# Optimization experiments

Measured on AMD Instinct MI355X. Metric: run time of the kernel, lower is better.

The kernel has to match this reference:

```python
import jax, jax.numpy as jnp
import numpy as np

B, N, HD, U = 2, 512, 64, 128  # batch, nodes, h_dim, mlp width


def _init(key, shape):
    return jax.random.normal(key, shape, dtype=jnp.float32) / np.sqrt(shape[0]).astype(np.float32)


def setup_inputs() -> dict:
    key = jax.random.key(0)
    ks = jax.random.split(key, 12)
    x = jax.random.normal(ks[0], (B, N, 3), dtype=jnp.float32)
    h = jax.random.normal(ks[1], (B, N, HD), dtype=jnp.float32)
    p = {}
    p['We1'] = _init(ks[2], (1 + 2 * HD, U)); p['be1'] = jnp.zeros((U,), jnp.float32)
    p['We2'] = _init(ks[3], (U, U));          p['be2'] = jnp.zeros((U,), jnp.float32)
    p['Winf'] = _init(ks[4], (U, 1));         p['binf'] = jnp.zeros((1,), jnp.float32)
    p['Wx1'] = _init(ks[5], (U, U));          p['bx1'] = jnp.zeros((U,), jnp.float32)
    p['Wx2'] = _init(ks[6], (U, U));          p['bx2'] = jnp.zeros((U,), jnp.float32)
    p['Wx3'] = _init(ks[7], (U, 1));          p['bx3'] = jnp.zeros((1,), jnp.float32)
    p['Wh1'] = _init(ks[8], (U + HD, U));     p['bh1'] = jnp.zeros((U,), jnp.float32)
    p['Wh2'] = _init(ks[9], (U, U));          p['bh2'] = jnp.zeros((U,), jnp.float32)
    p['Wout'] = _init(ks[10], (U, HD));       p['bout'] = jnp.zeros((HD,), jnp.float32)
    return {'x': x, 'h': h, **p}


def _mlp2(t, W1, b1, W2, b2):
    # hk.nets.MLP([U, U], activation=elu), activate_final=False
    return jax.nn.elu(t @ W1 + b1) @ W2 + b2


def reference(x, h, We1, be1, We2, be2, Winf, binf, Wx1, bx1, Wx2, bx2, Wx3, bx3, Wh1, bh1, Wh2, bh2, Wout, bout):
    Bn, Nn, _ = x.shape
    hd = h.shape[-1]
    mask = 1.0 - jnp.eye(Nn, dtype=x.dtype)  # zero the i==j diagonal
    # diff[b,i,j] = x[b,j] - x[b,i]  (matches x - x[:, None] in the original)
    diff = (x[:, None, :, :] - x[:, :, None, :]) * mask[None, :, :, None]  # [B,N,N,3]
    sq = jnp.sum(diff * diff, axis=-1)
    norms = jnp.sqrt(jnp.where(mask > 0, sq, 1.0)) * mask  # safe sqrt; diag exactly 0
    # h_combos[b,i,j] = concat(h[b,j], h[b,i])
    h_j = jnp.broadcast_to(h[:, None, :, :], (Bn, Nn, Nn, hd))
    h_i = jnp.broadcast_to(h[:, :, None, :], (Bn, Nn, Nn, hd))
    feat = jnp.concatenate([norms[..., None], h_j, h_i], axis=-1)  # [B,N,N,1+2*hd]
    m_ij = _mlp2(feat, We1, be1, We2, be2) * mask[None, :, :, None]  # [B,N,N,U]
    e = jax.nn.sigmoid(m_ij @ Winf + binf)[..., 0] * mask            # [B,N,N]
    m_i = jnp.einsum('bijd,bij->bid', m_ij, e)                       # [B,N,U]
    # phi_x: MLP(activate_final=True) then Linear(1)
    hid = jax.nn.elu(jax.nn.elu(m_ij @ Wx1 + bx1) @ Wx2 + bx2)
    phi_x_out = (hid @ Wx3 + bx3)[..., 0] * mask                     # [B,N,N]
    shift = jnp.einsum('bijd,bij->bid', diff, phi_x_out) / (Nn - 1)  # [B,N,3]
    h_new = _mlp2(jnp.concatenate([m_i, h], axis=-1), Wh1, bh1, Wh2, bh2) @ Wout + bout
    return (x + shift, h_new)
```

## Files before the change

kernel.cpp:

```cpp
#include <hip/hip_runtime.h>
#include <math.h>


#define BB    2
#define NN    512
#define HDIM  64
#define UDIM  128
#define JT    64
#define NTILE (NN / JT)
#define FP    72
#define PP    136

typedef float f32x4 __attribute__((ext_vector_type(4)));
typedef short s16x8 __attribute__((ext_vector_type(8)));

__device__ __forceinline__ ushort f2bf(float f) {
    union { float f; unsigned u; } v; v.f = f;
    return (ushort)((v.u + 0x7FFFu + ((v.u >> 16) & 1u)) >> 16);
}
__device__ __forceinline__ float bf2f(ushort s) {
    union { unsigned u; float f; } v; v.u = ((unsigned)s) << 16; return v.f;
}
__device__ __forceinline__ unsigned pk2(float lo, float hi) {
    unsigned r;
    asm("v_cvt_pk_bf16_f32 %0, %1, %2" : "=v"(r) : "v"(lo), "v"(hi));
    return r;
}
__device__ __forceinline__ f32x4 MFMA(s16x8 a, s16x8 b, f32x4 c) {
    return __builtin_amdgcn_mfma_f32_16x16x32_bf16(a, b, c, 0, 0, 0);
}
__device__ __forceinline__ float eluf(float v) { return v > 0.f ? v : __expf(v) - 1.f; }

__device__ __forceinline__ void load_wfrags(const float* __restrict__ W, int q, int uc0,
                                            s16x8 (&dst)[4][2]) {
#pragma unroll
    for (int s = 0; s < 4; ++s)
#pragma unroll
        for (int n = 0; n < 2; ++n) {
            s16x8 r;
#pragma unroll
            for (int ii = 0; ii < 8; ++ii)
                r[ii] = (short)f2bf(W[(32 * s + 8 * q + ii) * UDIM + uc0 + n]);
            dst[s][n] = r;
        }
}

template <int KSTEPS, int PITCH>
__device__ __forceinline__ void gemm_P(const ushort* __restrict__ P, const s16x8 (&wB)[KSTEPS][2],
                                       int l15, int q, f32x4 (&acc)[4][2]) {
#pragma unroll
    for (int s = 0; s < KSTEPS; ++s) {
        s16x8 a[4];
#pragma unroll
        for (int m = 0; m < 4; ++m)
            a[m] = *(const s16x8*)(P + (16 * m + l15) * PITCH + 32 * s + 8 * q);
#pragma unroll
        for (int m = 0; m < 4; ++m) {
            acc[m][0] = MFMA(a[m], wB[s][0], acc[m][0]);
            acc[m][1] = MFMA(a[m], wB[s][1], acc[m][1]);
        }
    }
}

template <bool ELU>
__device__ __forceinline__ void store_P(ushort* __restrict__ P, const f32x4 (&v)[4][2],
                                        int q, int uc0) {
#pragma unroll
    for (int m = 0; m < 4; ++m)
#pragma unroll
        for (int r = 0; r < 4; ++r) {
            const int row = 16 * m + 4 * q + r;
            float a = v[m][0][r], c = v[m][1][r];
            if (ELU) { a = eluf(a); c = eluf(c); }
            *(unsigned*)(P + row * PP + uc0) = pk2(a, c);
        }
}

__global__ __launch_bounds__(256, 2) void egnn_mfma(
    const float* __restrict__ x, const float* __restrict__ h,
    const float* __restrict__ We1, const float* __restrict__ be1,
    const float* __restrict__ We2, const float* __restrict__ be2,
    const float* __restrict__ Winf, const float* __restrict__ binf,
    const float* __restrict__ Wx1, const float* __restrict__ bx1,
    const float* __restrict__ Wx2, const float* __restrict__ bx2,
    const float* __restrict__ Wx3, const float* __restrict__ bx3,
    const float* __restrict__ Wh1, const float* __restrict__ bh1,
    const float* __restrict__ Wh2, const float* __restrict__ bh2,
    const float* __restrict__ Wout, const float* __restrict__ bout,
    float* __restrict__ out) {
    __shared__ ushort F[JT][FP];
    __shared__ ushort P1[JT][PP];
    __shared__ ushort P2[JT][PP];
    __shared__ float normL[JT];
    __shared__ float diffL[JT][3];
    __shared__ float rpartE[4][JT];
    __shared__ float rpartP[4][JT];
    __shared__ float eL[JT];
    __shared__ float bias1L[UDIM];
    __shared__ float WinfL[UDIM], Wx3L[UDIM];
    __shared__ float catL[UDIM + HDIM];
    __shared__ float th1[UDIM], th2[UDIM];

    const int bi = blockIdx.x;
    const int b  = bi >> 9;
    const int i  = bi & (NN - 1);
    const int tid  = threadIdx.x;
    const int lane = tid & 63;
    const int w    = tid >> 6;
    const int l15  = lane & 15;
    const int q    = lane >> 4;
    const int uc0  = 32 * w + 2 * l15;

    s16x8 wB1[2][2];
#pragma unroll
    for (int s = 0; s < 2; ++s)
#pragma unroll
        for (int n = 0; n < 2; ++n) {
            s16x8 r;
#pragma unroll
            for (int ii = 0; ii < 8; ++ii)
                r[ii] = (short)f2bf(We1[(1 + 32 * s + 8 * q + ii) * UDIM + uc0 + n]);
            wB1[s][n] = r;
        }
    s16x8 wB2[4][2], wB3[4][2], wB4[4][2];
    load_wfrags(We2, q, uc0, wB2);
    load_wfrags(Wx1, q, uc0, wB3);
    load_wfrags(Wx2, q, uc0, wB4);

    if (tid < UDIM) {
        WinfL[tid] = Winf[tid];
        Wx3L[tid]  = Wx3[tid];
        float s = be1[tid];
        const float* hi = &h[(b * NN + i) * HDIM];
#pragma unroll 8
        for (int k = 0; k < HDIM; ++k)
            s = fmaf(hi[k], We1[(1 + HDIM + k) * UDIM + tid], s);
        bias1L[tid] = s;
    }
    const float w0n0 = We1[uc0], w0n1 = We1[uc0 + 1];
    const float b2n0 = be2[uc0], b2n1 = be2[uc0 + 1];
    const float bqn0 = bx1[uc0], bqn1 = bx1[uc0 + 1];
    const float brn0 = bx2[uc0], brn1 = bx2[uc0 + 1];
    const float binf0 = binf[0], bx30 = bx3[0];
    const float xi0 = x[(b * NN + i) * 3 + 0];
    const float xi1 = x[(b * NN + i) * 3 + 1];
    const float xi2 = x[(b * NN + i) * 3 + 2];
    __syncthreads();
    const float b1n0 = bias1L[uc0], b1n1 = bias1L[uc0 + 1];

    float mi0 = 0.f, mi1 = 0.f;
    float sh0 = 0.f, sh1 = 0.f, sh2 = 0.f;

    for (int t = 0; t < NTILE; ++t) {
        const int j0 = t * JT;
        __syncthreads();

        {
            const int jr = tid >> 2, k0 = (tid & 3) * 16;
            const float* hp = &h[(b * NN + j0 + jr) * HDIM + k0];
            const float4 f0 = *(const float4*)hp;
            const float4 f1 = *(const float4*)(hp + 4);
            const float4 f2 = *(const float4*)(hp + 8);
            const float4 f3 = *(const float4*)(hp + 12);
            uint4 pv0, pv1;
            pv0.x = pk2(f0.x, f0.y); pv0.y = pk2(f0.z, f0.w);
            pv0.z = pk2(f1.x, f1.y); pv0.w = pk2(f1.z, f1.w);
            pv1.x = pk2(f2.x, f2.y); pv1.y = pk2(f2.z, f2.w);
            pv1.z = pk2(f3.x, f3.y); pv1.w = pk2(f3.z, f3.w);
            *(uint4*)&F[jr][k0]     = pv0;
            *(uint4*)&F[jr][k0 + 8] = pv1;
        }
        if (tid < JT) {
            const int j = j0 + tid;
            float d0 = x[(b * NN + j) * 3 + 0] - xi0;
            float d1 = x[(b * NN + j) * 3 + 1] - xi1;
            float d2 = x[(b * NN + j) * 3 + 2] - xi2;
            if (j == i) { d0 = 0.f; d1 = 0.f; d2 = 0.f; }
            diffL[tid][0] = d0; diffL[tid][1] = d1; diffL[tid][2] = d2;
            normL[tid] = (j == i) ? 0.f : sqrtf(d0 * d0 + d1 * d1 + d2 * d2);
        }
        __syncthreads();

        f32x4 acc[4][2];
#pragma unroll
        for (int m = 0; m < 4; ++m)
#pragma unroll
            for (int r = 0; r < 4; ++r) {
                const float nrm = normL[16 * m + 4 * q + r];
                acc[m][0][r] = fmaf(nrm, w0n0, b1n0);
                acc[m][1][r] = fmaf(nrm, w0n1, b1n1);
            }
        gemm_P<2, FP>(&F[0][0], wB1, l15, q, acc);
        store_P<true>(&P1[0][0], acc, q, uc0);
        __syncthreads();

        f32x4 macc[4][2];
#pragma unroll
        for (int m = 0; m < 4; ++m)
#pragma unroll
            for (int r = 0; r < 4; ++r) { macc[m][0][r] = b2n0; macc[m][1][r] = b2n1; }
        gemm_P<4, PP>(&P1[0][0], wB2, l15, q, macc);
#pragma unroll
        for (int m = 0; m < 4; ++m)
#pragma unroll
            for (int r = 0; r < 4; ++r)
                if (j0 + 16 * m + 4 * q + r == i) { macc[m][0][r] = 0.f; macc[m][1][r] = 0.f; }
        store_P<false>(&P2[0][0], macc, q, uc0);
        __syncthreads();

        {
            const int jj = tid & 63, sl = tid >> 6;
            const ushort* pr = &P2[jj][32 * sl];
            float p = 0.f;
#pragma unroll
            for (int cc = 0; cc < 4; ++cc) {
                const s16x8 mv = *(const s16x8*)(pr + 8 * cc);
#pragma unroll
                for (int c = 0; c < 8; ++c)
                    p = fmaf(bf2f((ushort)mv[c]), WinfL[32 * sl + 8 * cc + c], p);
            }
            rpartE[sl][jj] = p;
        }
        f32x4 qacc[4][2];
#pragma unroll
        for (int m = 0; m < 4; ++m)
#pragma unroll
            for (int r = 0; r < 4; ++r) { qacc[m][0][r] = bqn0; qacc[m][1][r] = bqn1; }
        gemm_P<4, PP>(&P2[0][0], wB3, l15, q, qacc);
        store_P<true>(&P1[0][0], qacc, q, uc0);
        __syncthreads();

        if (tid < JT) {
            float s = rpartE[0][tid] + rpartE[1][tid] + rpartE[2][tid] + rpartE[3][tid];
            float e = 1.f / (1.f + __expf(-(s + binf0)));
            if (j0 + tid == i) e = 0.f;
            eL[tid] = e;
        }
        f32x4 racc[4][2];
#pragma unroll
        for (int m = 0; m < 4; ++m)
#pragma unroll
            for (int r = 0; r < 4; ++r) { racc[m][0][r] = brn0; racc[m][1][r] = brn1; }
        gemm_P<4, PP>(&P1[0][0], wB4, l15, q, racc);
        store_P<true>(&P2[0][0], racc, q, uc0);
        __syncthreads();

        {
            const int jj = tid & 63, sl = tid >> 6;
            const ushort* pr = &P2[jj][32 * sl];
            float p = 0.f;
#pragma unroll
            for (int cc = 0; cc < 4; ++cc) {
                const s16x8 mv = *(const s16x8*)(pr + 8 * cc);
#pragma unroll
                for (int c = 0; c < 8; ++c)
                    p = fmaf(bf2f((ushort)mv[c]), Wx3L[32 * sl + 8 * cc + c], p);
            }
            rpartP[sl][jj] = p;
        }
#pragma unroll
        for (int m = 0; m < 4; ++m)
#pragma unroll
            for (int r = 0; r < 4; ++r) {
                const float e = eL[16 * m + 4 * q + r];
                mi0 = fmaf(macc[m][0][r], e, mi0);
                mi1 = fmaf(macc[m][1][r], e, mi1);
            }
        __syncthreads();

        if (tid < JT) {
            float s = rpartP[0][tid] + rpartP[1][tid] + rpartP[2][tid] + rpartP[3][tid];
            s += bx30;
            if (j0 + tid == i) s = 0.f;
            float v0 = diffL[tid][0] * s;
            float v1 = diffL[tid][1] * s;
            float v2 = diffL[tid][2] * s;
#pragma unroll
            for (int d = 1; d < 64; d <<= 1) {
                v0 += __shfl_xor(v0, d);
                v1 += __shfl_xor(v1, d);
                v2 += __shfl_xor(v2, d);
            }
            sh0 += v0; sh1 += v1; sh2 += v2;
        }
    }

    __syncthreads();
    {
        float v0 = mi0, v1 = mi1;
        v0 += __shfl_xor(v0, 16); v0 += __shfl_xor(v0, 32);
        v1 += __shfl_xor(v1, 16); v1 += __shfl_xor(v1, 32);
        if (lane < 16) {
            catL[uc0]     = v0;
            catL[uc0 + 1] = v1;
        }
    }
    if (tid >= 128 && tid < 128 + HDIM)
        catL[UDIM + tid - 128] = h[(b * NN + i) * HDIM + (tid - 128)];
    if (tid == 0) {
        const float inv = 1.f / (float)(NN - 1);
        out[(b * NN + i) * 3 + 0] = x[(b * NN + i) * 3 + 0] + sh0 * inv;
        out[(b * NN + i) * 3 + 1] = x[(b * NN + i) * 3 + 1] + sh1 * inv;
        out[(b * NN + i) * 3 + 2] = x[(b * NN + i) * 3 + 2] + sh2 * inv;
    }
    __syncthreads();

    if (tid < UDIM) {
        float s = bh1[tid];
        for (int k = 0; k < UDIM + HDIM; ++k) s = fmaf(catL[k], Wh1[k * UDIM + tid], s);
        th1[tid] = eluf(s);
    }
    __syncthreads();
    if (tid < UDIM) {
        float s = bh2[tid];
        for (int k = 0; k < UDIM; ++k) s = fmaf(th1[k], Wh2[k * UDIM + tid], s);
        th2[tid] = s;
    }
    __syncthreads();
    if (tid < HDIM) {
        float s = bout[tid];
        for (int k = 0; k < UDIM; ++k) s = fmaf(th2[k], Wout[k * HDIM + tid], s);
        out[BB * NN * 3 + (b * NN + i) * HDIM + tid] = s;
    }
}

extern "C" void kernel_launch(void* const* d_in, const int* in_sizes, int n_in,
                              void* d_out, int out_size, void* d_ws, size_t ws_size,
                              hipStream_t stream) {
    const float* x    = (const float*)d_in[0];
    const float* h    = (const float*)d_in[1];
    const float* We1  = (const float*)d_in[2];
    const float* be1  = (const float*)d_in[3];
    const float* We2  = (const float*)d_in[4];
    const float* be2  = (const float*)d_in[5];
    const float* Winf = (const float*)d_in[6];
    const float* binf = (const float*)d_in[7];
    const float* Wx1  = (const float*)d_in[8];
    const float* bx1  = (const float*)d_in[9];
    const float* Wx2  = (const float*)d_in[10];
    const float* bx2  = (const float*)d_in[11];
    const float* Wx3  = (const float*)d_in[12];
    const float* bx3  = (const float*)d_in[13];
    const float* Wh1  = (const float*)d_in[14];
    const float* bh1  = (const float*)d_in[15];
    const float* Wh2  = (const float*)d_in[16];
    const float* bh2  = (const float*)d_in[17];
    const float* Wout = (const float*)d_in[18];
    const float* bout = (const float*)d_in[19];
    float* out = (float*)d_out;

    hipLaunchKernelGGL(egnn_mfma, dim3(BB * NN), dim3(256), 0, stream,
                       x, h, We1, be1, We2, be2, Winf, binf, Wx1, bx1, Wx2, bx2,
                       Wx3, bx3, Wh1, bh1, Wh2, bh2, Wout, bout, out);
}
```

Before: 141.2 us.

## Double-buffer j-tiles, fold norm and Winf projection into MFMA, cut barriers

Prefetches the next tile's h rows and coordinate differences into registers during the current tile's GEMMs, then writes them into a double-buffered LDS tile. The norm term moves into an extra K-step of the first MFMA GEMM, and the Winf edge projection rides on wave 0's Wx1 GEMM as an extra MFMA column. The Wx3 projection is reduced in registers with shuffles instead of a separate LDS pass. This removes two barriers per tile and the scalar bf16 dot-product loops. In exchange it adds register pressure, makes wave 0 do more work than the others, and rounds the norm to bf16.

After: 418.4 us. 196% more time.

```diff
diff --git a/kernel.cpp b/kernel.cpp
--- a/kernel.cpp
+++ b/kernel.cpp
@@ -18,9 +18,6 @@
     union { float f; unsigned u; } v; v.f = f;
     return (ushort)((v.u + 0x7FFFu + ((v.u >> 16) & 1u)) >> 16);
 }
-__device__ __forceinline__ float bf2f(ushort s) {
-    union { unsigned u; float f; } v; v.u = ((unsigned)s) << 16; return v.f;
-}
 __device__ __forceinline__ unsigned pk2(float lo, float hi) {
     unsigned r;
     asm("v_cvt_pk_bf16_f32 %0, %1, %2" : "=v"(r) : "v"(lo), "v"(hi));
@@ -45,9 +42,11 @@
         }
 }
 
-template <int KSTEPS, int PITCH>
-__device__ __forceinline__ void gemm_P(const ushort* __restrict__ P, const s16x8 (&wB)[KSTEPS][2],
-                                       int l15, int q, f32x4 (&acc)[4][2]) {
+template <int KSTEPS, int PITCH, bool EXTRA>
+__device__ __forceinline__ void gemm_P(const ushort* __restrict__ P,
+                                       const s16x8 (&wB)[KSTEPS][2], const s16x8* wE,
+                                       int l15, int q, f32x4 (&acc)[4][2], f32x4* eacc) {
+    __builtin_amdgcn_s_setprio(1);
 #pragma unroll
     for (int s = 0; s < KSTEPS; ++s) {
         s16x8 a[4];
@@ -58,8 +57,10 @@
         for (int m = 0; m < 4; ++m) {
             acc[m][0] = MFMA(a[m], wB[s][0], acc[m][0]);
             acc[m][1] = MFMA(a[m], wB[s][1], acc[m][1]);
-        }
-    }
+            if (EXTRA) eacc[m] = MFMA(a[m], wE[s], eacc[m]);
+        }
+    }
+    __builtin_amdgcn_s_setprio(0);
 }
 
 template <bool ELU>
@@ -88,16 +89,14 @@
     const float* __restrict__ Wh2, const float* __restrict__ bh2,
     const float* __restrict__ Wout, const float* __restrict__ bout,
     float* __restrict__ out) {
-    __shared__ ushort F[JT][FP];
+    __shared__ ushort F[2][JT + 1][FP];
     __shared__ ushort P1[JT][PP];
     __shared__ ushort P2[JT][PP];
-    __shared__ float normL[JT];
-    __shared__ float diffL[JT][3];
-    __shared__ float rpartE[4][JT];
-    __shared__ float rpartP[4][JT];
+    __shared__ float diffL[2][JT][3];
+    __shared__ float rp3[4][JT];
     __shared__ float eL[JT];
     __shared__ float bias1L[UDIM];
-    __shared__ float WinfL[UDIM], Wx3L[UDIM];
+    __shared__ float shiftL[3];
     __shared__ float catL[UDIM + HDIM];
     __shared__ float th1[UDIM], th2[UDIM];
 
@@ -110,8 +109,9 @@
     const int l15  = lane & 15;
     const int q    = lane >> 4;
     const int uc0  = 32 * w + 2 * l15;
-
-    s16x8 wB1[2][2];
+    const int jr   = tid >> 2, k0 = (tid & 3) * 16;
+
+    s16x8 wB1[3][2];
 #pragma unroll
     for (int s = 0; s < 2; ++s)
 #pragma unroll
@@ -122,14 +122,29 @@
                 r[ii] = (short)f2bf(We1[(1 + 32 * s + 8 * q + ii) * UDIM + uc0 + n]);
             wB1[s][n] = r;
         }
+#pragma unroll
+    for (int n = 0; n < 2; ++n) {
+        s16x8 r;
+#pragma unroll
+        for (int ii = 0; ii < 8; ++ii)
+            r[ii] = (q == 0 && ii == 0) ? (short)f2bf(We1[uc0 + n]) : (short)0;
+        wB1[2][n] = r;
+    }
     s16x8 wB2[4][2], wB3[4][2], wB4[4][2];
     load_wfrags(We2, q, uc0, wB2);
     load_wfrags(Wx1, q, uc0, wB3);
     load_wfrags(Wx2, q, uc0, wB4);
+    s16x8 wE[4];
+#pragma unroll
+    for (int s = 0; s < 4; ++s) {
+        s16x8 r;
+#pragma unroll
+        for (int ii = 0; ii < 8; ++ii)
+            r[ii] = (l15 == 0) ? (short)f2bf(Winf[32 * s + 8 * q + ii]) : (short)0;
+        wE[s] = r;
+    }
 
     if (tid < UDIM) {
-        WinfL[tid] = Winf[tid];
-        Wx3L[tid]  = Wx3[tid];
         float s = be1[tid];
         const float* hi = &h[(b * NN + i) * HDIM];
 #pragma unroll 8
@@ -137,60 +152,77 @@
             s = fmaf(hi[k], We1[(1 + HDIM + k) * UDIM + tid], s);
         bias1L[tid] = s;
     }
-    const float w0n0 = We1[uc0], w0n1 = We1[uc0 + 1];
     const float b2n0 = be2[uc0], b2n1 = be2[uc0 + 1];
     const float bqn0 = bx1[uc0], bqn1 = bx1[uc0 + 1];
     const float brn0 = bx2[uc0], brn1 = bx2[uc0 + 1];
+    const float wx30 = Wx3[uc0], wx31 = Wx3[uc0 + 1];
     const float binf0 = binf[0], bx30 = bx3[0];
     const float xi0 = x[(b * NN + i) * 3 + 0];
     const float xi1 = x[(b * NN + i) * 3 + 1];
     const float xi2 = x[(b * NN + i) * 3 + 2];
-    __syncthreads();
-    const float b1n0 = bias1L[uc0], b1n1 = bias1L[uc0 + 1];
-
-    float mi0 = 0.f, mi1 = 0.f;
-    float sh0 = 0.f, sh1 = 0.f, sh2 = 0.f;
-
-    for (int t = 0; t < NTILE; ++t) {
-        const int j0 = t * JT;
-        __syncthreads();
-
-        {
-            const int jr = tid >> 2, k0 = (tid & 3) * 16;
-            const float* hp = &h[(b * NN + j0 + jr) * HDIM + k0];
-            const float4 f0 = *(const float4*)hp;
-            const float4 f1 = *(const float4*)(hp + 4);
-            const float4 f2 = *(const float4*)(hp + 8);
-            const float4 f3 = *(const float4*)(hp + 12);
-            uint4 pv0, pv1;
-            pv0.x = pk2(f0.x, f0.y); pv0.y = pk2(f0.z, f0.w);
-            pv0.z = pk2(f1.x, f1.y); pv0.w = pk2(f1.z, f1.w);
-            pv1.x = pk2(f2.x, f2.y); pv1.y = pk2(f2.z, f2.w);
-            pv1.z = pk2(f3.x, f3.y); pv1.w = pk2(f3.z, f3.w);
-            *(uint4*)&F[jr][k0]     = pv0;
-            *(uint4*)&F[jr][k0 + 8] = pv1;
-        }
+
+    if (tid < 2 * FP) {
+        const int f = tid / FP, c = tid % FP;
+        F[f][JT][c] = 0;
+    }
+    {
+        const float* hp = &h[(b * NN + jr) * HDIM + k0];
+        const float4 f0 = *(const float4*)hp;
+        const float4 f1 = *(const float4*)(hp + 4);
+        const float4 f2 = *(const float4*)(hp + 8);
+        const float4 f3 = *(const float4*)(hp + 12);
+        uint4 pv0, pv1;
+        pv0.x = pk2(f0.x, f0.y); pv0.y = pk2(f0.z, f0.w);
+        pv0.z = pk2(f1.x, f1.y); pv0.w = pk2(f1.z, f1.w);
+        pv1.x = pk2(f2.x, f2.y); pv1.y = pk2(f2.z, f2.w);
+        pv1.z = pk2(f3.x, f3.y); pv1.w = pk2(f3.z, f3.w);
+        *(uint4*)&F[0][jr][k0]     = pv0;
+        *(uint4*)&F[0][jr][k0 + 8] = pv1;
         if (tid < JT) {
-            const int j = j0 + tid;
+            const int j = tid;
             float d0 = x[(b * NN + j) * 3 + 0] - xi0;
             float d1 = x[(b * NN + j) * 3 + 1] - xi1;
             float d2 = x[(b * NN + j) * 3 + 2] - xi2;
             if (j == i) { d0 = 0.f; d1 = 0.f; d2 = 0.f; }
-            diffL[tid][0] = d0; diffL[tid][1] = d1; diffL[tid][2] = d2;
-            normL[tid] = (j == i) ? 0.f : sqrtf(d0 * d0 + d1 * d1 + d2 * d2);
-        }
-        __syncthreads();
-
+            diffL[0][tid][0] = d0; diffL[0][tid][1] = d1; diffL[0][tid][2] = d2;
+            const float nrm = sqrtf(d0 * d0 + d1 * d1 + d2 * d2);
+            s16x8 nr = {(short)f2bf(nrm), 0, 0, 0, 0, 0, 0, 0};
+            *(s16x8*)&F[0][tid][64] = nr;
+        }
+    }
+    __syncthreads();
+    const float b1n0 = bias1L[uc0], b1n1 = bias1L[uc0 + 1];
+
+    float mi0 = 0.f, mi1 = 0.f;
+    float shc = 0.f;
+
+    for (int t = 0; t < NTILE; ++t) {
+        const int cur = t & 1, nxt = cur ^ 1;
+        const int j0 = t * JT;
+        const bool more = (t + 1 < NTILE);
+
+        float4 hv0, hv1, hv2, hv3;
+        float sxd0 = 0.f, sxd1 = 0.f, sxd2 = 0.f;
+        if (more) {
+            const float* hp = &h[(b * NN + j0 + JT + jr) * HDIM + k0];
+            hv0 = *(const float4*)hp;
+            hv1 = *(const float4*)(hp + 4);
+            hv2 = *(const float4*)(hp + 8);
+            hv3 = *(const float4*)(hp + 12);
+            if (tid < JT) {
+                const int j = j0 + JT + tid;
+                sxd0 = x[(b * NN + j) * 3 + 0] - xi0;
+                sxd1 = x[(b * NN + j) * 3 + 1] - xi1;
+                sxd2 = x[(b * NN + j) * 3 + 2] - xi2;
+                if (j == i) { sxd0 = 0.f; sxd1 = 0.f; sxd2 = 0.f; }
+            }
+        }
         f32x4 acc[4][2];
 #pragma unroll
         for (int m = 0; m < 4; ++m)
 #pragma unroll
-            for (int r = 0; r < 4; ++r) {
-                const float nrm = normL[16 * m + 4 * q + r];
-                acc[m][0][r] = fmaf(nrm, w0n0, b1n0);
-                acc[m][1][r] = fmaf(nrm, w0n1, b1n1);
-            }
-        gemm_P<2, FP>(&F[0][0], wB1, l15, q, acc);
+            for (int r = 0; r < 4; ++r) { acc[m][0][r] = b1n0; acc[m][1][r] = b1n1; }
+        gemm_P<3, FP, false>(&F[cur][0][0], wB1, nullptr, l15, q, acc, nullptr);
         store_P<true>(&P1[0][0], acc, q, uc0);
         __syncthreads();
 
@@ -199,7 +231,7 @@
         for (int m = 0; m < 4; ++m)
 #pragma unroll
             for (int r = 0; r < 4; ++r) { macc[m][0][r] = b2n0; macc[m][1][r] = b2n1; }
-        gemm_P<4, PP>(&P1[0][0], wB2, l15, q, macc);
+        gemm_P<4, PP, false>(&P1[0][0], wB2, nullptr, l15, q, macc, nullptr);
 #pragma unroll
         for (int m = 0; m < 4; ++m)
 #pragma unroll
@@ -208,56 +240,50 @@
         store_P<false>(&P2[0][0], macc, q, uc0);
         __syncthreads();
 
-        {
-            const int jj = tid & 63, sl = tid >> 6;
-            const ushort* pr = &P2[jj][32 * sl];
-            float p = 0.f;
-#pragma unroll
-            for (int cc = 0; cc < 4; ++cc) {
-                const s16x8 mv = *(const s16x8*)(pr + 8 * cc);
-#pragma unroll
-                for (int c = 0; c < 8; ++c)
-                    p = fmaf(bf2f((ushort)mv[c]), WinfL[32 * sl + 8 * cc + c], p);
-            }
-            rpartE[sl][jj] = p;
-        }
         f32x4 qacc[4][2];
 #pragma unroll
         for (int m = 0; m < 4; ++m)
 #pragma unroll
             for (int r = 0; r < 4; ++r) { qacc[m][0][r] = bqn0; qacc[m][1][r] = bqn1; }
-        gemm_P<4, PP>(&P2[0][0], wB3, l15, q, qacc);
+        if (w == 0) {
+            f32x4 eacc[4];
+#pragma unroll
+            for (int m = 0; m < 4; ++m)
+#pragma unroll
+                for (int r = 0; r < 4; ++r) eacc[m][r] = 0.f;
+            gemm_P<4, PP, true>(&P2[0][0], wB3, wE, l15, q, qacc, eacc);
+            if (l15 == 0) {
+#pragma unroll
+                for (int m = 0; m < 4; ++m)
+#pragma unroll
+                    for (int r = 0; r < 4; ++r) {
+                        const int row = 16 * m + 4 * q + r;
+                        float e = 1.f / (1.f + __expf(-(eacc[m][r] + binf0)));
+                        if (j0 + row == i) e = 0.f;
+                        eL[row] = e;
+                    }
+            }
+        } else {
+            gemm_P<4, PP, false>(&P2[0][0], wB3, nullptr, l15, q, qacc, nullptr);
+        }
         store_P<true>(&P1[0][0], qacc, q, uc0);
+        if (more) {
+            uint4 pv0, pv1;
+            pv0.x = pk2(hv0.x, hv0.y); pv0.y = pk2(hv0.z, hv0.w);
+            pv0.z = pk2(hv1.x, hv1.y); pv0.w = pk2(hv1.z, hv1.w);
+            pv1.x = pk2(hv2.x, hv2.y); pv1.y = pk2(hv2.z, hv2.w);
+            pv1.z = pk2(hv3.x, hv3.y); pv1.w = pk2(hv3.z, hv3.w);
+            *(uint4*)&F[nxt][jr][k0]     = pv0;
+            *(uint4*)&F[nxt][jr][k0 + 8] = pv1;
+            if (tid < JT) {
+                diffL[nxt][tid][0] = sxd0; diffL[nxt][tid][1] = sxd1; diffL[nxt][tid][2] = sxd2;
+                const float nrm = sqrtf(sxd0 * sxd0 + sxd1 * sxd1 + sxd2 * sxd2);
+                s16x8 nr = {(short)f2bf(nrm), 0, 0, 0, 0, 0, 0, 0};
+                *(s16x8*)&F[nxt][tid][64] = nr;
+            }
+        }
         __syncthreads();
 
-        if (tid < JT) {
-            float s = rpartE[0][tid] + rpartE[1][tid] + rpartE[2][tid] + rpartE[3][tid];
-            float e = 1.f / (1.f + __expf(-(s + binf0)));
-            if (j0 + tid == i) e = 0.f;
-            eL[tid] = e;
-        }
-        f32x4 racc[4][2];
-#pragma unroll
-        for (int m = 0; m < 4; ++m)
-#pragma unroll
-            for (int r = 0; r < 4; ++r) { racc[m][0][r] = brn0; racc[m][1][r] = brn1; }
-        gemm_P<4, PP>(&P1[0][0], wB4, l15, q, racc);
-        store_P<true>(&P2[0][0], racc, q, uc0);
-        __syncthreads();
-
-        {
-            const int jj = tid & 63, sl = tid >> 6;
-            const ushort* pr = &P2[jj][32 * sl];
-            float p = 0.f;
-#pragma unroll
-            for (int cc = 0; cc < 4; ++cc) {
-                const s16x8 mv = *(const s16x8*)(pr + 8 * cc);
-#pragma unroll
-                for (int c = 0; c < 8; ++c)
-                    p = fmaf(bf2f((ushort)mv[c]), Wx3L[32 * sl + 8 * cc + c], p);
-            }
-            rpartP[sl][jj] = p;
-        }
 #pragma unroll
         for (int m = 0; m < 4; ++m)
 #pragma unroll
@@ -266,26 +292,38 @@
                 mi0 = fmaf(macc[m][0][r], e, mi0);
                 mi1 = fmaf(macc[m][1][r], e, mi1);
             }
+        f32x4 racc[4][2];
+#pragma unroll
+        for (int m = 0; m < 4; ++m)
+#pragma unroll
+            for (int r = 0; r < 4; ++r) { racc[m][0][r] = brn0; racc[m][1][r] = brn1; }
+        gemm_P<4, PP, false>(&P1[0][0], wB4, nullptr, l15, q, racc, nullptr);
+#pragma unroll
+        for (int m = 0; m < 4; ++m)
+#pragma unroll
+            for (int r = 0; r < 4; ++r) {
+                float p = eluf(racc[m][0][r]) * wx30 + eluf(racc[m][1][r]) * wx31;
+                p += __shfl_xor(p, 1);
+                p += __shfl_xor(p, 2);
+                p += __shfl_xor(p, 4);
+                p += __shfl_xor(p, 8);
+                if (l15 == 0) {
+                    float s = p + (w == 0 ? bx30 : 0.f);
+                    rp3[w][16 * m + 4 * q + r] = s;
+                }
+            }
         __syncthreads();
 
-        if (tid < JT) {
-            float s = rpartP[0][tid] + rpartP[1][tid] + rpartP[2][tid] + rpartP[3][tid];
-            s += bx30;
-            if (j0 + tid == i) s = 0.f;
-            float v0 = diffL[tid][0] * s;
-            float v1 = diffL[tid][1] * s;
-            float v2 = diffL[tid][2] * s;
-#pragma unroll
-            for (int d = 1; d < 64; d <<= 1) {
-                v0 += __shfl_xor(v0, d);
-                v1 += __shfl_xor(v1, d);
-                v2 += __shfl_xor(v2, d);
-            }
-            sh0 += v0; sh1 += v1; sh2 += v2;
-        }
-    }
-
-    __syncthreads();
+        if (w < 3) {
+            const int j = lane;
+            float tot = rp3[0][j] + rp3[1][j] + rp3[2][j] + rp3[3][j];
+            float val = tot * diffL[cur][j][w];
+#pragma unroll
+            for (int d = 1; d < 64; d <<= 1) val += __shfl_xor(val, d);
+            shc += val;
+        }
+    }
+
     {
         float v0 = mi0, v1 = mi1;
         v0 += __shfl_xor(v0, 16); v0 += __shfl_xor(v0, 32);
@@ -297,13 +335,15 @@
     }
     if (tid >= 128 && tid < 128 + HDIM)
         catL[UDIM + tid - 128] = h[(b * NN + i) * HDIM + (tid - 128)];
+    if (w < 3 && lane == 0) shiftL[w] = shc;
+    __syncthreads();
+
     if (tid == 0) {
         const float inv = 1.f / (float)(NN - 1);
-        out[(b * NN + i) * 3 + 0] = x[(b * NN + i) * 3 + 0] + sh0 * inv;
-        out[(b * NN + i) * 3 + 1] = x[(b * NN + i) * 3 + 1] + sh1 * inv;
-        out[(b * NN + i) * 3 + 2] = x[(b * NN + i) * 3 + 2] + sh2 * inv;
-    }
-    __syncthreads();
+        out[(b * NN + i) * 3 + 0] = x[(b * NN + i) * 3 + 0] + shiftL[0] * inv;
+        out[(b * NN + i) * 3 + 1] = x[(b * NN + i) * 3 + 1] + shiftL[1] * inv;
+        out[(b * NN + i) * 3 + 2] = x[(b * NN + i) * 3 + 2] + shiftL[2] * inv;
+    }
 
     if (tid < UDIM) {
         float s = bh1[tid];
```

## Double-buffer j-tile inputs, fuse phi_x final projection into registers, drop syncs

Applied to the files above, without the earlier changes.

Double-buffers the per-tile h features and x diffs in shared memory, so the next tile's global loads are issued mid-iteration and written after the last GEMM. This removes the two barriers at the top of each tile. The phi_x output projection (Wx3) is now done directly on the GEMM accumulators in registers instead of storing to P2 and re-reading bf16. The edge gate is broadcast with shuffles rather than through shared memory. Per-iteration barriers drop, at the cost of more registers and extra shared memory for the buffers, and s_setprio is raised around the MFMA loops.

Result: slower. 193.4 us (+36.9%).

```diff
diff --git a/kernel.cpp b/kernel.cpp
--- a/kernel.cpp
+++ b/kernel.cpp
@@ -18,14 +18,14 @@
     union { float f; unsigned u; } v; v.f = f;
     return (ushort)((v.u + 0x7FFFu + ((v.u >> 16) & 1u)) >> 16);
 }
-__device__ __forceinline__ float bf2f(ushort s) {
-    union { unsigned u; float f; } v; v.u = ((unsigned)s) << 16; return v.f;
-}
 __device__ __forceinline__ unsigned pk2(float lo, float hi) {
     unsigned r;
     asm("v_cvt_pk_bf16_f32 %0, %1, %2" : "=v"(r) : "v"(lo), "v"(hi));
     return r;
 }
+__device__ __forceinline__ float bf2f(ushort s) {
+    union { unsigned u; float f; } v; v.u = ((unsigned)s) << 16; return v.f;
+}
 __device__ __forceinline__ f32x4 MFMA(s16x8 a, s16x8 b, f32x4 c) {
     return __builtin_amdgcn_mfma_f32_16x16x32_bf16(a, b, c, 0, 0, 0);
 }
@@ -48,6 +48,7 @@
 template <int KSTEPS, int PITCH>
 __device__ __forceinline__ void gemm_P(const ushort* __restrict__ P, const s16x8 (&wB)[KSTEPS][2],
                                        int l15, int q, f32x4 (&acc)[4][2]) {
+    __builtin_amdgcn_s_setprio(1);
 #pragma unroll
     for (int s = 0; s < KSTEPS; ++s) {
         s16x8 a[4];
@@ -60,6 +61,7 @@
             acc[m][1] = MFMA(a[m], wB[s][1], acc[m][1]);
         }
     }
+    __builtin_amdgcn_s_setprio(0);
 }
 
 template <bool ELU>
@@ -88,16 +90,15 @@
     const float* __restrict__ Wh2, const float* __restrict__ bh2,
     const float* __restrict__ Wout, const float* __restrict__ bout,
     float* __restrict__ out) {
-    __shared__ ushort F[JT][FP];
+    __shared__ ushort F[2][JT][FP];
     __shared__ ushort P1[JT][PP];
     __shared__ ushort P2[JT][PP];
-    __shared__ float normL[JT];
-    __shared__ float diffL[JT][3];
+    __shared__ float normL[2][JT];
+    __shared__ float diffL[2][JT][3];
     __shared__ float rpartE[4][JT];
-    __shared__ float rpartP[4][JT];
-    __shared__ float eL[JT];
     __shared__ float bias1L[UDIM];
-    __shared__ float WinfL[UDIM], Wx3L[UDIM];
+    __shared__ float WinfL[UDIM];
+    __shared__ float shiftL[4][3];
     __shared__ float catL[UDIM + HDIM];
     __shared__ float th1[UDIM], th2[UDIM];
 
@@ -110,6 +111,7 @@
     const int l15  = lane & 15;
     const int q    = lane >> 4;
     const int uc0  = 32 * w + 2 * l15;
+    const int jr   = tid >> 2, k0 = (tid & 3) * 16;
 
     s16x8 wB1[2][2];
 #pragma unroll
@@ -129,7 +131,6 @@
 
     if (tid < UDIM) {
         WinfL[tid] = Winf[tid];
-        Wx3L[tid]  = Wx3[tid];
         float s = be1[tid];
         const float* hi = &h[(b * NN + i) * HDIM];
 #pragma unroll 8
@@ -141,56 +142,56 @@
     const float b2n0 = be2[uc0], b2n1 = be2[uc0 + 1];
     const float bqn0 = bx1[uc0], bqn1 = bx1[uc0 + 1];
     const float brn0 = bx2[uc0], brn1 = bx2[uc0 + 1];
+    const float wx30 = Wx3[uc0], wx31 = Wx3[uc0 + 1];
     const float binf0 = binf[0], bx30 = bx3[0];
     const float xi0 = x[(b * NN + i) * 3 + 0];
     const float xi1 = x[(b * NN + i) * 3 + 1];
     const float xi2 = x[(b * NN + i) * 3 + 2];
-    __syncthreads();
-    const float b1n0 = bias1L[uc0], b1n1 = bias1L[uc0 + 1];
-
-    float mi0 = 0.f, mi1 = 0.f;
-    float sh0 = 0.f, sh1 = 0.f, sh2 = 0.f;
-
-    for (int t = 0; t < NTILE; ++t) {
-        const int j0 = t * JT;
-        __syncthreads();
-
-        {
-            const int jr = tid >> 2, k0 = (tid & 3) * 16;
-            const float* hp = &h[(b * NN + j0 + jr) * HDIM + k0];
-            const float4 f0 = *(const float4*)hp;
-            const float4 f1 = *(const float4*)(hp + 4);
-            const float4 f2 = *(const float4*)(hp + 8);
-            const float4 f3 = *(const float4*)(hp + 12);
-            uint4 pv0, pv1;
-            pv0.x = pk2(f0.x, f0.y); pv0.y = pk2(f0.z, f0.w);
-            pv0.z = pk2(f1.x, f1.y); pv0.w = pk2(f1.z, f1.w);
-            pv1.x = pk2(f2.x, f2.y); pv1.y = pk2(f2.z, f2.w);
-            pv1.z = pk2(f3.x, f3.y); pv1.w = pk2(f3.z, f3.w);
-            *(uint4*)&F[jr][k0]     = pv0;
-            *(uint4*)&F[jr][k0 + 8] = pv1;
-        }
+
+    {
+        const float* hp = &h[(b * NN + jr) * HDIM + k0];
+        const float4 f0 = *(const float4*)hp;
+        const float4 f1 = *(const float4*)(hp + 4);
+        const float4 f2 = *(const float4*)(hp + 8);
+        const float4 f3 = *(const float4*)(hp + 12);
+        uint4 pv0, pv1;
+        pv0.x = pk2(f0.x, f0.y); pv0.y = pk2(f0.z, f0.w);
+        pv0.z = pk2(f1.x, f1.y); pv0.w = pk2(f1.z, f1.w);
+        pv1.x = pk2(f2.x, f2.y); pv1.y = pk2(f2.z, f2.w);
+        pv1.z = pk2(f3.x, f3.y); pv1.w = pk2(f3.z, f3.w);
+        *(uint4*)&F[0][jr][k0]     = pv0;
+        *(uint4*)&F[0][jr][k0 + 8] = pv1;
         if (tid < JT) {
-            const int j = j0 + tid;
+            const int j = tid;
             float d0 = x[(b * NN + j) * 3 + 0] - xi0;
             float d1 = x[(b * NN + j) * 3 + 1] - xi1;
             float d2 = x[(b * NN + j) * 3 + 2] - xi2;
             if (j == i) { d0 = 0.f; d1 = 0.f; d2 = 0.f; }
-            diffL[tid][0] = d0; diffL[tid][1] = d1; diffL[tid][2] = d2;
-            normL[tid] = (j == i) ? 0.f : sqrtf(d0 * d0 + d1 * d1 + d2 * d2);
-        }
-        __syncthreads();
+            diffL[0][tid][0] = d0; diffL[0][tid][1] = d1; diffL[0][tid][2] = d2;
+            normL[0][tid] = sqrtf(d0 * d0 + d1 * d1 + d2 * d2);
+        }
+    }
+    __syncthreads();
+    const float b1n0 = bias1L[uc0], b1n1 = bias1L[uc0 + 1];
+
+    float mi0 = 0.f, mi1 = 0.f;
+    float sh0 = 0.f, sh1 = 0.f, sh2 = 0.f;
+
+    for (int t = 0; t < NTILE; ++t) {
+        const int cur = t & 1, nxt = cur ^ 1;
+        const int j0 = t * JT;
+        const bool more = (t + 1 < NTILE);
 
         f32x4 acc[4][2];
 #pragma unroll
         for (int m = 0; m < 4; ++m)
 #pragma unroll
             for (int r = 0; r < 4; ++r) {
-                const float nrm = normL[16 * m + 4 * q + r];
+                const float nrm = normL[cur][16 * m + 4 * q + r];
                 acc[m][0][r] = fmaf(nrm, w0n0, b1n0);
                 acc[m][1][r] = fmaf(nrm, w0n1, b1n1);
             }
-        gemm_P<2, FP>(&F[0][0], wB1, l15, q, acc);
+        gemm_P<2, FP>(&F[cur][0][0], wB1, l15, q, acc);
         store_P<true>(&P1[0][0], acc, q, uc0);
         __syncthreads();
 
@@ -230,62 +231,70 @@
         store_P<true>(&P1[0][0], qacc, q, uc0);
         __syncthreads();
 
-        if (tid < JT) {
-            float s = rpartE[0][tid] + rpartE[1][tid] + rpartE[2][tid] + rpartE[3][tid];
-            float e = 1.f / (1.f + __expf(-(s + binf0)));
-            if (j0 + tid == i) e = 0.f;
-            eL[tid] = e;
-        }
+        float4 hv0, hv1, hv2, hv3;
+        float sxd0 = 0.f, sxd1 = 0.f, sxd2 = 0.f;
+        if (more) {
+            const float* hp = &h[(b * NN + j0 + JT + jr) * HDIM + k0];
+            hv0 = *(const float4*)hp;
+            hv1 = *(const float4*)(hp + 4);
+            hv2 = *(const float4*)(hp + 8);
+            hv3 = *(const float4*)(hp + 12);
+            if (tid < JT) {
+                const int j = j0 + JT + tid;
+                sxd0 = x[(b * NN + j) * 3 + 0] - xi0;
+                sxd1 = x[(b * NN + j) * 3 + 1] - xi1;
+                sxd2 = x[(b * NN + j) * 3 + 2] - xi2;
+                if (j == i) { sxd0 = 0.f; sxd1 = 0.f; sxd2 = 0.f; }
+            }
+        }
+        float ev;
+        {
+            const float es = rpartE[0][lane] + rpartE[1][lane] +
+                             rpartE[2][lane] + rpartE[3][lane];
+            ev = 1.f / (1.f + __expf(-(es + binf0)));
+        }
+#pragma unroll
+        for (int m = 0; m < 4; ++m)
+#pragma unroll
+            for (int r = 0; r < 4; ++r) {
+                const float e = __shfl(ev, 16 * m + 4 * q + r);
+                mi0 = fmaf(macc[m][0][r], e, mi0);
+                mi1 = fmaf(macc[m][1][r], e, mi1);
+            }
         f32x4 racc[4][2];
 #pragma unroll
         for (int m = 0; m < 4; ++m)
 #pragma unroll
             for (int r = 0; r < 4; ++r) { racc[m][0][r] = brn0; racc[m][1][r] = brn1; }
         gemm_P<4, PP>(&P1[0][0], wB4, l15, q, racc);
-        store_P<true>(&P2[0][0], racc, q, uc0);
+        if (more) {
+            uint4 pv0, pv1;
+            pv0.x = pk2(hv0.x, hv0.y); pv0.y = pk2(hv0.z, hv0.w);
+            pv0.z = pk2(hv1.x, hv1.y); pv0.w = pk2(hv1.z, hv1.w);
+            pv1.x = pk2(hv2.x, hv2.y); pv1.y = pk2(hv2.z, hv2.w);
+            pv1.z = pk2(hv3.x, hv3.y); pv1.w = pk2(hv3.z, hv3.w);
+            *(uint4*)&F[nxt][jr][k0]     = pv0;
+            *(uint4*)&F[nxt][jr][k0 + 8] = pv1;
+            if (tid < JT) {
+                diffL[nxt][tid][0] = sxd0; diffL[nxt][tid][1] = sxd1; diffL[nxt][tid][2] = sxd2;
+                normL[nxt][tid] = sqrtf(sxd0 * sxd0 + sxd1 * sxd1 + sxd2 * sxd2);
+            }
+        }
+#pragma unroll
+        for (int m = 0; m < 4; ++m)
+#pragma unroll
+            for (int r = 0; r < 4; ++r) {
+                const int row = 16 * m + 4 * q + r;
+                float p = eluf(racc[m][0][r]) * wx30 + eluf(racc[m][1][r]) * wx31;
+                if (w == 0 && l15 == 0) p += bx30;
+                if (j0 + row == i) p = 0.f;
+                sh0 = fmaf(p, diffL[cur][row][0], sh0);
+                sh1 = fmaf(p, diffL[cur][row][1], sh1);
+                sh2 = fmaf(p, diffL[cur][row][2], sh2);
+            }
         __syncthreads();
-
-        {
-            const int jj = tid & 63, sl = tid >> 6;
-            const ushort* pr = &P2[jj][32 * sl];
-            float p = 0.f;
-#pragma unroll
-            for (int cc = 0; cc < 4; ++cc) {
-                const s16x8 mv = *(const s16x8*)(pr + 8 * cc);
-#pragma unroll
-                for (int c = 0; c < 8; ++c)
-                    p = fmaf(bf2f((ushort)mv[c]), Wx3L[32 * sl + 8 * cc + c], p);
-            }
-            rpartP[sl][jj] = p;
-        }
-#pragma unroll
-        for (int m = 0; m < 4; ++m)
-#pragma unroll
-            for (int r = 0; r < 4; ++r) {
-                const float e = eL[16 * m + 4 * q + r];
-                mi0 = fmaf(macc[m][0][r], e, mi0);
-                mi1 = fmaf(macc[m][1][r], e, mi1);
-            }
-        __syncthreads();
-
-        if (tid < JT) {
-            float s = rpartP[0][tid] + rpartP[1][tid] + rpartP[2][tid] + rpartP[3][tid];
-            s += bx30;
-            if (j0 + tid == i) s = 0.f;
-            float v0 = diffL[tid][0] * s;
-            float v1 = diffL[tid][1] * s;
-            float v2 = diffL[tid][2] * s;
-#pragma unroll
-            for (int d = 1; d < 64; d <<= 1) {
-                v0 += __shfl_xor(v0, d);
-                v1 += __shfl_xor(v1, d);
-                v2 += __shfl_xor(v2, d);
-            }
-            sh0 += v0; sh1 += v1; sh2 += v2;
-        }
-    }
-
-    __syncthreads();
+    }
+
     {
         float v0 = mi0, v1 = mi1;
         v0 += __shfl_xor(v0, 16); v0 += __shfl_xor(v0, 32);
@@ -295,15 +304,24 @@
             catL[uc0 + 1] = v1;
         }
     }
+    {
+#pragma unroll
+        for (int d = 1; d < 64; d <<= 1) {
+            sh0 += __shfl_xor(sh0, d);
+            sh1 += __shfl_xor(sh1, d);
+            sh2 += __shfl_xor(sh2, d);
+        }
+        if (lane == 0) { shiftL[w][0] = sh0; shiftL[w][1] = sh1; shiftL[w][2] = sh2; }
+    }
     if (tid >= 128 && tid < 128 + HDIM)
         catL[UDIM + tid - 128] = h[(b * NN + i) * HDIM + (tid - 128)];
-    if (tid == 0) {
+    __syncthreads();
+
+    if (tid < 3) {
         const float inv = 1.f / (float)(NN - 1);
-        out[(b * NN + i) * 3 + 0] = x[(b * NN + i) * 3 + 0] + sh0 * inv;
-        out[(b * NN + i) * 3 + 1] = x[(b * NN + i) * 3 + 1] + sh1 * inv;
-        out[(b * NN + i) * 3 + 2] = x[(b * NN + i) * 3 + 2] + sh2 * inv;
-    }
-    __syncthreads();
+        const float s = shiftL[0][tid] + shiftL[1][tid] + shiftL[2][tid] + shiftL[3][tid];
+        out[(b * NN + i) * 3 + tid] = x[(b * NN + i) * 3 + tid] + s * inv;
+    }
 
     if (tid < UDIM) {
         float s = bh1[tid];
```
